# Performance work log

Hardware: AMD Instinct MI355X
Metric: run time of the kernel (lower is better)

The kernel has to match this reference:

```python
import jax, jax.numpy as jnp
import numpy as np

OBJ_COOR = 5.0
OBJ_CONFI = 1.0
NO_OBJ_CONFI = 0.5
IMG_CLASS_WEIGHT = 1.0
LOG_CLAMP = -100.0  # torch.F.binary_cross_entropy clamps log terms at -100


def setup_inputs() -> dict:
    key = jax.random.key(0)
    k1, k2, k3, k4, k5, k6 = jax.random.split(key, 6)
    B, A, H, W, C = 64, 9, 128, 128, 1000
    objects = jax.random.uniform(k1, (B, A, H, W), dtype=jnp.float32)  # predicted probs
    scores = jax.random.normal(k2, (B, C), dtype=jnp.float32)
    locs = jax.random.normal(k3, (B, A, 4, H, W), dtype=jnp.float32)
    label = jax.random.randint(k4, (B,), 0, C)
    # gt: channel 0 is exact 0/1 objectness mask, channels 1:5 are target coords
    mask = jax.random.bernoulli(k5, 0.05, (B, A, 1, H, W)).astype(jnp.float32)
    coords = jax.random.uniform(k6, (B, A, 4, H, W), dtype=jnp.float32)
    gt = jnp.concatenate([mask, coords], axis=2)  # [B,A,5,H,W]
    return {"objects": objects, "scores": scores, "locs": locs, "label": label, "gt": gt}


def reference(objects, scores, locs, label, gt):
    B = objects.shape[0]
    m = gt[:, :, 0]  # [B,A,H,W] exact 0.0 / 1.0 mask
    log_p = jnp.clip(jnp.log(objects), LOG_CLAMP)
    log_1mp = jnp.clip(jnp.log1p(-objects), LOG_CLAMP)
    # BCE(p, 0) = -log(1-p); BCE(p, 1) = -log(p); masked sums over all cells
    no_obj_confi_loss = jnp.sum((1.0 - m) * (-log_1mp))
    obj_confi_loss = jnp.sum(m * (-log_p))
    sq = jnp.sum((locs[:, :, 0:4] - gt[:, :, 1:5]) ** 2, axis=2)  # [B,A,H,W]
    obj_coor_loss = jnp.sum(m * sq)
    # image classification cross entropy (mean over batch)
    logp = jax.nn.log_softmax(scores, axis=-1)
    img_class_loss = -jnp.mean(logp[jnp.arange(B), label])
    return IMG_CLASS_WEIGHT * img_class_loss + (
        NO_OBJ_CONFI * no_obj_confi_loss
        + OBJ_CONFI * obj_confi_loss
        + OBJ_COOR * obj_coor_loss
    ) / B
```

## Files before the change

### kernel.cpp

```cpp
#include <hip/hip_runtime.h>

static constexpr int HW4 = 4096;
static constexpr float LOGCLAMP = -100.0f;


__device__ __forceinline__ void stage16(const float4* g, float4* l) {
    __builtin_amdgcn_global_load_lds(
        (const __attribute__((address_space(1))) void*)g,
        (__attribute__((address_space(3))) void*)l,
        16, 0, 0);
}

__global__ __launch_bounds__(256) void main_loss_kernel(
    const float4* __restrict__ objects,
    const float4* __restrict__ locs,
    const float4* __restrict__ gt,
    float* __restrict__ ws)
{
    __shared__ float4 lds[10 * 256];

    const int b    = blockIdx.x;
    const int tid  = threadIdx.x;
    const int wb   = tid & ~63;

    const int ba = b >> 2;
    const float4* gtb = gt   + ba * 5 * HW4;
    const float4* lcb = locs + ba * 4 * HW4;

    float s_noobj = 0.0f, s_obj = 0.0f, s_coor = 0.0f;

    #pragma unroll 1
    for (int r = 0; r < 4; ++r) {
        const int chunk = b * 4 + r;
        const int c4    = chunk & 15;
        const int off   = c4 * 256;

        stage16(objects + chunk * 256 + tid, lds + 0 * 256 + wb);
        stage16(gtb + 0 * HW4 + off + tid,   lds + 1 * 256 + wb);
        stage16(gtb + 1 * HW4 + off + tid,   lds + 2 * 256 + wb);
        stage16(gtb + 2 * HW4 + off + tid,   lds + 3 * 256 + wb);
        stage16(gtb + 3 * HW4 + off + tid,   lds + 4 * 256 + wb);
        stage16(gtb + 4 * HW4 + off + tid,   lds + 5 * 256 + wb);
        stage16(lcb + 0 * HW4 + off + tid,   lds + 6 * 256 + wb);
        stage16(lcb + 1 * HW4 + off + tid,   lds + 7 * 256 + wb);
        stage16(lcb + 2 * HW4 + off + tid,   lds + 8 * 256 + wb);
        stage16(lcb + 3 * HW4 + off + tid,   lds + 9 * 256 + wb);

        asm volatile("s_waitcnt vmcnt(0)" ::: "memory");
        __syncthreads();

        const float4 o  = lds[0 * 256 + tid];
        const float4 m  = lds[1 * 256 + tid];
        const float4 g0 = lds[2 * 256 + tid];
        const float4 g1 = lds[3 * 256 + tid];
        const float4 g2 = lds[4 * 256 + tid];
        const float4 g3 = lds[5 * 256 + tid];
        const float4 l0 = lds[6 * 256 + tid];
        const float4 l1 = lds[7 * 256 + tid];
        const float4 l2 = lds[8 * 256 + tid];
        const float4 l3 = lds[9 * 256 + tid];

        {
            const float d0 = l0.x - g0.x, d1 = l1.x - g1.x,
                        d2 = l2.x - g2.x, d3 = l3.x - g3.x;
            const float sq = d0 * d0 + d1 * d1 + d2 * d2 + d3 * d3;
            const float lp  = fmaxf(__logf(o.x),        LOGCLAMP);
            const float l1m = fmaxf(__logf(1.0f - o.x), LOGCLAMP);
            s_noobj -= (1.0f - m.x) * l1m;
            s_obj   -= m.x * lp;
            s_coor  += m.x * sq;
        }
        {
            const float d0 = l0.y - g0.y, d1 = l1.y - g1.y,
                        d2 = l2.y - g2.y, d3 = l3.y - g3.y;
            const float sq = d0 * d0 + d1 * d1 + d2 * d2 + d3 * d3;
            const float lp  = fmaxf(__logf(o.y),        LOGCLAMP);
            const float l1m = fmaxf(__logf(1.0f - o.y), LOGCLAMP);
            s_noobj -= (1.0f - m.y) * l1m;
            s_obj   -= m.y * lp;
            s_coor  += m.y * sq;
        }
        {
            const float d0 = l0.z - g0.z, d1 = l1.z - g1.z,
                        d2 = l2.z - g2.z, d3 = l3.z - g3.z;
            const float sq = d0 * d0 + d1 * d1 + d2 * d2 + d3 * d3;
            const float lp  = fmaxf(__logf(o.z),        LOGCLAMP);
            const float l1m = fmaxf(__logf(1.0f - o.z), LOGCLAMP);
            s_noobj -= (1.0f - m.z) * l1m;
            s_obj   -= m.z * lp;
            s_coor  += m.z * sq;
        }
        {
            const float d0 = l0.w - g0.w, d1 = l1.w - g1.w,
                        d2 = l2.w - g2.w, d3 = l3.w - g3.w;
            const float sq = d0 * d0 + d1 * d1 + d2 * d2 + d3 * d3;
            const float lp  = fmaxf(__logf(o.w),        LOGCLAMP);
            const float l1m = fmaxf(__logf(1.0f - o.w), LOGCLAMP);
            s_noobj -= (1.0f - m.w) * l1m;
            s_obj   -= m.w * lp;
            s_coor  += m.w * sq;
        }

        __syncthreads();
    }

    #pragma unroll
    for (int off = 32; off > 0; off >>= 1) {
        s_noobj += __shfl_down(s_noobj, off, 64);
        s_obj   += __shfl_down(s_obj,   off, 64);
        s_coor  += __shfl_down(s_coor,  off, 64);
    }

    __shared__ float red[3][4];
    const int lane = threadIdx.x & 63;
    const int wid  = threadIdx.x >> 6;
    if (lane == 0) {
        red[0][wid] = s_noobj;
        red[1][wid] = s_obj;
        red[2][wid] = s_coor;
    }
    __syncthreads();
    if (threadIdx.x == 0) {
        atomicAdd(&ws[0], red[0][0] + red[0][1] + red[0][2] + red[0][3]);
        atomicAdd(&ws[1], red[1][0] + red[1][1] + red[1][2] + red[1][3]);
        atomicAdd(&ws[2], red[2][0] + red[2][1] + red[2][2] + red[2][3]);
    }
}

__global__ __launch_bounds__(256) void class_loss_kernel(
    const float* __restrict__ scores,
    const int*   __restrict__ label,
    float* __restrict__ ws)
{
    const int b = blockIdx.x;
    const float* row = scores + b * 1000;

    float mx = -INFINITY;
    for (int i = threadIdx.x; i < 1000; i += 256) mx = fmaxf(mx, row[i]);
    #pragma unroll
    for (int off = 32; off > 0; off >>= 1) mx = fmaxf(mx, __shfl_down(mx, off, 64));

    __shared__ float smax[4];
    const int lane = threadIdx.x & 63;
    const int wid  = threadIdx.x >> 6;
    if (lane == 0) smax[wid] = mx;
    __syncthreads();
    mx = fmaxf(fmaxf(smax[0], smax[1]), fmaxf(smax[2], smax[3]));

    float se = 0.0f;
    for (int i = threadIdx.x; i < 1000; i += 256) se += __expf(row[i] - mx);
    #pragma unroll
    for (int off = 32; off > 0; off >>= 1) se += __shfl_down(se, off, 64);

    __shared__ float ssum[4];
    if (lane == 0) ssum[wid] = se;
    __syncthreads();
    if (threadIdx.x == 0) {
        se = ssum[0] + ssum[1] + ssum[2] + ssum[3];
        const float logp = row[label[b]] - mx - __logf(se);
        atomicAdd(&ws[3], -logp * (1.0f / 64.0f));
    }
}

__global__ void finalize_kernel(const float* __restrict__ ws, float* __restrict__ out)
{
    out[0] = ws[3] + (0.5f * ws[0] + 1.0f * ws[1] + 5.0f * ws[2]) * (1.0f / 64.0f);
}

extern "C" void kernel_launch(void* const* d_in, const int* in_sizes, int n_in,
                              void* d_out, int out_size, void* d_ws, size_t ws_size,
                              hipStream_t stream)
{
    const float* objects = (const float*)d_in[0];
    const float* scores  = (const float*)d_in[1];
    const float* locs    = (const float*)d_in[2];
    const int*   label   = (const int*)d_in[3];
    const float* gt      = (const float*)d_in[4];
    float* ws  = (float*)d_ws;
    float* out = (float*)d_out;

    hipMemsetAsync(ws, 0, 4 * sizeof(float), stream);

    main_loss_kernel<<<2304, 256, 0, stream>>>(
        (const float4*)objects, (const float4*)locs, (const float4*)gt, ws);
    class_loss_kernel<<<64, 256, 0, stream>>>(scores, label, ws);
    finalize_kernel<<<1, 1, 0, stream>>>(ws, out);
}
```

Measured before the change: 127.4 us.

## Double-buffer LDS staging with async prefetch and drop block barriers

```diff
diff --git a/kernel.cpp b/kernel.cpp
--- a/kernel.cpp
+++ b/kernel.cpp
@@ -1,6 +1,8 @@
 #include <hip/hip_runtime.h>
 
-static constexpr int HW4 = 4096;
+static constexpr int HW4   = 4096;
+static constexpr int CHUNK = 128;
+static constexpr int ROUNDS = 8;
 static constexpr float LOGCLAMP = -100.0f;
 
 
@@ -11,54 +13,70 @@
         16, 0, 0);
 }
 
-__global__ __launch_bounds__(256) void main_loss_kernel(
+__global__ __launch_bounds__(128) void main_loss_kernel(
     const float4* __restrict__ objects,
     const float4* __restrict__ locs,
     const float4* __restrict__ gt,
     float* __restrict__ ws)
 {
-    __shared__ float4 lds[10 * 256];
-
-    const int b    = blockIdx.x;
-    const int tid  = threadIdx.x;
-    const int wb   = tid & ~63;
-
-    const int ba = b >> 2;
-    const float4* gtb = gt   + ba * 5 * HW4;
-    const float4* lcb = locs + ba * 4 * HW4;
+    __shared__ float4 lds[2][10][CHUNK];
+
+    const int b   = blockIdx.x;
+    const int tid = threadIdx.x;
+    const int wb  = tid & ~63;
+
+    const int ba  = b >> 2;
+    const int sub = b & 3;
+
+    const float4* pO  = objects + ba * HW4     + sub * 1024;
+    const float4* gtb = gt      + ba * 5 * HW4 + sub * 1024;
+    const float4* lcb = locs    + ba * 4 * HW4 + sub * 1024;
+
+    auto stage_round = [&](int r) {
+        const int off = r * CHUNK + tid;
+        float4* dst = &lds[r & 1][0][wb];
+        stage16(pO  + off,            dst + 0 * CHUNK);
+        stage16(gtb + 0 * HW4 + off,  dst + 1 * CHUNK);
+        stage16(gtb + 1 * HW4 + off,  dst + 2 * CHUNK);
+        stage16(gtb + 2 * HW4 + off,  dst + 3 * CHUNK);
+        stage16(gtb + 3 * HW4 + off,  dst + 4 * CHUNK);
+        stage16(gtb + 4 * HW4 + off,  dst + 5 * CHUNK);
+        stage16(lcb + 0 * HW4 + off,  dst + 6 * CHUNK);
+        stage16(lcb + 1 * HW4 + off,  dst + 7 * CHUNK);
+        stage16(lcb + 2 * HW4 + off,  dst + 8 * CHUNK);
+        stage16(lcb + 3 * HW4 + off,  dst + 9 * CHUNK);
+    };
 
     float s_noobj = 0.0f, s_obj = 0.0f, s_coor = 0.0f;
 
-    #pragma unroll 1
-    for (int r = 0; r < 4; ++r) {
-        const int chunk = b * 4 + r;
-        const int c4    = chunk & 15;
-        const int off   = c4 * 256;
-
-        stage16(objects + chunk * 256 + tid, lds + 0 * 256 + wb);
-        stage16(gtb + 0 * HW4 + off + tid,   lds + 1 * 256 + wb);
-        stage16(gtb + 1 * HW4 + off + tid,   lds + 2 * 256 + wb);
-        stage16(gtb + 2 * HW4 + off + tid,   lds + 3 * 256 + wb);
-        stage16(gtb + 3 * HW4 + off + tid,   lds + 4 * 256 + wb);
-        stage16(gtb + 4 * HW4 + off + tid,   lds + 5 * 256 + wb);
-        stage16(lcb + 0 * HW4 + off + tid,   lds + 6 * 256 + wb);
-        stage16(lcb + 1 * HW4 + off + tid,   lds + 7 * 256 + wb);
-        stage16(lcb + 2 * HW4 + off + tid,   lds + 8 * 256 + wb);
-        stage16(lcb + 3 * HW4 + off + tid,   lds + 9 * 256 + wb);
-
-        asm volatile("s_waitcnt vmcnt(0)" ::: "memory");
-        __syncthreads();
-
-        const float4 o  = lds[0 * 256 + tid];
-        const float4 m  = lds[1 * 256 + tid];
-        const float4 g0 = lds[2 * 256 + tid];
-        const float4 g1 = lds[3 * 256 + tid];
-        const float4 g2 = lds[4 * 256 + tid];
-        const float4 g3 = lds[5 * 256 + tid];
-        const float4 l0 = lds[6 * 256 + tid];
-        const float4 l1 = lds[7 * 256 + tid];
-        const float4 l2 = lds[8 * 256 + tid];
-        const float4 l3 = lds[9 * 256 + tid];
+    stage_round(0);
+    stage_round(1);
+
+    #pragma unroll
+    for (int r = 0; r < ROUNDS; ++r) {
+        if (r < ROUNDS - 1)
+            asm volatile("s_waitcnt vmcnt(10)" ::: "memory");
+        else
+            asm volatile("s_waitcnt vmcnt(0)" ::: "memory");
+        __builtin_amdgcn_sched_barrier(0);
+
+        const int buf = r & 1;
+        const float4 o  = lds[buf][0][tid];
+        const float4 m  = lds[buf][1][tid];
+        const float4 g0 = lds[buf][2][tid];
+        const float4 g1 = lds[buf][3][tid];
+        const float4 g2 = lds[buf][4][tid];
+        const float4 g3 = lds[buf][5][tid];
+        const float4 l0 = lds[buf][6][tid];
+        const float4 l1 = lds[buf][7][tid];
+        const float4 l2 = lds[buf][8][tid];
+        const float4 l3 = lds[buf][9][tid];
+
+        if (r < ROUNDS - 2) {
+            asm volatile("s_waitcnt lgkmcnt(0)" ::: "memory");
+            __builtin_amdgcn_sched_barrier(0);
+            stage_round(r + 2);
+        }
 
         {
             const float d0 = l0.x - g0.x, d1 = l1.x - g1.x,
@@ -100,8 +118,6 @@
             s_obj   -= m.w * lp;
             s_coor  += m.w * sq;
         }
-
-        __syncthreads();
     }
 
     #pragma unroll
@@ -111,19 +127,19 @@
         s_coor  += __shfl_down(s_coor,  off, 64);
     }
 
-    __shared__ float red[3][4];
-    const int lane = threadIdx.x & 63;
-    const int wid  = threadIdx.x >> 6;
+    __shared__ float red[3][2];
+    const int lane = tid & 63;
+    const int wid  = tid >> 6;
     if (lane == 0) {
         red[0][wid] = s_noobj;
         red[1][wid] = s_obj;
         red[2][wid] = s_coor;
     }
     __syncthreads();
-    if (threadIdx.x == 0) {
-        atomicAdd(&ws[0], red[0][0] + red[0][1] + red[0][2] + red[0][3]);
-        atomicAdd(&ws[1], red[1][0] + red[1][1] + red[1][2] + red[1][3]);
-        atomicAdd(&ws[2], red[2][0] + red[2][1] + red[2][2] + red[2][3]);
+    if (tid == 0) {
+        atomicAdd(&ws[0], red[0][0] + red[0][1]);
+        atomicAdd(&ws[1], red[1][0] + red[1][1]);
+        atomicAdd(&ws[2], red[2][0] + red[2][1]);
     }
 }
 
@@ -181,7 +197,7 @@
 
     hipMemsetAsync(ws, 0, 4 * sizeof(float), stream);
 
-    main_loss_kernel<<<2304, 256, 0, stream>>>(
+    main_loss_kernel<<<2304, 128, 0, stream>>>(
         (const float4*)objects, (const float4*)locs, (const float4*)gt, ws);
     class_loss_kernel<<<64, 256, 0, stream>>>(scores, label, ws);
     finalize_kernel<<<1, 1, 0, stream>>>(ws, out);
```

Measured after the change: 130.5 us. +2.4%, slower.
